# Kernel optimization log

Hardware: AMD Instinct MI355X
Metric: run time of the kernel (lower is better)

Reference implementation:

```python
import jax, jax.numpy as jnp
import numpy as np

C_IN, HIDDEN, C_OUT, N_NODE = 200, 128, 2, 200
BATCH = 512

def setup_inputs() -> dict:
    key = jax.random.key(0)
    k1, k2, k3, k4 = jax.random.split(key, 4)
    x = jax.random.normal(k1, (BATCH, N_NODE, C_IN), dtype=jnp.float32)
    adj = jax.random.randint(k2, (BATCH, N_NODE, N_NODE), 0, 2, dtype=jnp.int32)
    # GINConv MLPs (single Linear each); stored as [in, out]
    W1 = jax.random.normal(k3, (C_IN, HIDDEN), dtype=jnp.float32) / np.sqrt(C_IN)
    b1 = jnp.zeros((HIDDEN,), dtype=jnp.float32)
    W2 = jax.random.normal(k4, (HIDDEN, C_OUT), dtype=jnp.float32) / np.sqrt(HIDDEN)
    b2 = jnp.zeros((C_OUT,), dtype=jnp.float32)
    eps1 = jnp.zeros((), dtype=jnp.float32)  # train_eps=True, init 0
    eps2 = jnp.zeros((), dtype=jnp.float32)
    return {"x": x, "adj": adj, "W1": W1, "b1": b1, "W2": W2, "b2": b2, "eps1": eps1, "eps2": eps2}

def _gin_aggregate(adjf, h):
    # edge (b,i,j) sends h[b,i] to node j: agg[b,j] = sum_i adj[b,i,j]*h[b,i]
    return jnp.einsum('bij,bif->bjf', adjf, h)

def reference(x, adj, W1, b1, W2, b2, eps1, eps2):
    adjf = adj.astype(x.dtype)  # binary 0/1 adjacency [B,N,N]
    # GIN layer 1: nn((1+eps)*x + sum_neighbors(x)), then ReLU
    agg1 = _gin_aggregate(adjf, x)
    h = jax.nn.relu(((1.0 + eps1) * x + agg1) @ W1 + b1)
    # GIN layer 2
    agg2 = _gin_aggregate(adjf, h)
    out = ((1.0 + eps2) * h + agg2) @ W2 + b2  # [B,N,2]
    return out.mean(axis=-2)  # [B,2]
```

## Files before the change

### kernel.cpp

```cpp
#include <hip/hip_runtime.h>

#define BATCH 512
#define NNODE 200
#define CIN   200
#define HID   128
#define IPY   232
#define KCH   7

typedef __attribute__((ext_vector_type(4))) float  f32x4;
typedef __attribute__((ext_vector_type(4))) int    i32x4;
typedef __attribute__((ext_vector_type(8))) short  sh8;
typedef __attribute__((ext_vector_type(4))) short  sh4;
typedef __attribute__((ext_vector_type(8))) __bf16 bf16x8;

__device__ __forceinline__ short f2bf(float x) {
  union { float f; unsigned u; } v; v.f = x;
  unsigned r = v.u + 0x7FFFu + ((v.u >> 16) & 1u);
  return (short)(r >> 16);
}
__device__ __forceinline__ float bf2f(short s) {
  union { unsigned u; float f; } v; v.u = ((unsigned)(unsigned short)s) << 16;
  return v.f;
}
__device__ __forceinline__ f32x4 mfma16(sh8 a, sh8 b, f32x4 c) {
  return __builtin_amdgcn_mfma_f32_16x16x32_bf16(
      __builtin_bit_cast(bf16x8, a), __builtin_bit_cast(bf16x8, b), c, 0, 0, 0);
}
__device__ __forceinline__ f32x4 mfma16i(sh8 a, i32x4 b, f32x4 c) {
  return __builtin_amdgcn_mfma_f32_16x16x32_bf16(
      __builtin_bit_cast(bf16x8, a), __builtin_bit_cast(bf16x8, b), c, 0, 0, 0);
}
__device__ __forceinline__ i32x4 expand8(unsigned byte_) {
  i32x4 w;
#pragma unroll
  for (int h = 0; h < 4; ++h) {
    unsigned p = byte_ >> (2 * h);
    unsigned d = ((p & 1u) ? 0x3F80u : 0u) | ((p & 2u) ? 0x3F800000u : 0u);
    w[h] = (int)d;
  }
  return w;
}

__global__ __launch_bounds__(256) void k_prep(const float* __restrict__ W1,
                                              short* __restrict__ W1T) {
  const int idx = blockIdx.x * 256 + threadIdx.x;
  const int f = idx / IPY, c = idx - f * IPY;
  W1T[idx] = (c < CIN) ? f2bf(W1[(size_t)c * HID + f]) : (short)0;
}

__global__ __launch_bounds__(1024) void k_gin(const float* __restrict__ x,
                                              const int* __restrict__ adj,
                                              const short* __restrict__ W1Tg,
                                              const float* __restrict__ b1,
                                              const float* __restrict__ W2,
                                              const float* __restrict__ b2,
                                              const float* __restrict__ eps1p,
                                              const float* __restrict__ eps2p,
                                              float* __restrict__ out) {
  __shared__ __align__(16) short    ls_w1t[HID * IPY];
  __shared__ __align__(16) short    ls_slab[16 * IPY];
  __shared__ __align__(16) unsigned ls_bits[KCH * 224];
  __shared__ __align__(16) float    ls_deg[224];
  __shared__ __align__(16) float    ls_w2b1[384];
  __shared__               float    ls_part[13][2];

  const int b    = blockIdx.x;
  const int tid  = threadIdx.x;
  const int wave = tid >> 6, lane = tid & 63;
  const int lq   = lane >> 4, lm = lane & 15;
  const int* adjb = adj + (size_t)b * NNODE * NNODE;

  sh8 af[KCH];

  if (wave >= 13) {
    const int iw  = wave - 13;
    const int wd0 = iw * 2, wd1 = (iw == 2) ? 7 : iw * 2 + 2;
    const int jc3 = min(192 + lane, NNODE - 1);
    for (int wd = wd0; wd < wd1; ++wd) {
      const int tmax = (wd == 6) ? 8 : 32;
      unsigned w0 = 0, w1 = 0, w2 = 0, w3 = 0;
      for (int t8 = 0; t8 < tmax; t8 += 8) {
        int v0[8], v1[8], v2[8], v3[8];
#pragma unroll
        for (int rr = 0; rr < 8; ++rr) {
          const int* rp = adjb + (wd * 32 + t8 + rr) * NNODE;
          v0[rr] = rp[lane]; v1[rr] = rp[64 + lane];
          v2[rr] = rp[128 + lane]; v3[rr] = rp[jc3];
        }
#pragma unroll
        for (int rr = 0; rr < 8; ++rr) {
          const int t = t8 + rr;
          const unsigned b0 = (unsigned)v0[rr] & 1u;
          const unsigned b1_ = (unsigned)v1[rr] & 1u;
          const unsigned b2_ = (unsigned)v2[rr] & 1u;
          const unsigned b3_ = (lane < 8) ? ((unsigned)v3[rr] & 1u) : 0u;
          w0 |= b0 << t; w1 |= b1_ << t; w2 |= b2_ << t; w3 |= b3_ << t;
          const int dg = __popcll(__ballot(b0 != 0u)) + __popcll(__ballot(b1_ != 0u))
                       + __popcll(__ballot(b2_ != 0u)) + __popcll(__ballot(b3_ != 0u));
          if (lane == 0) ls_deg[wd * 32 + t] = (float)dg;
        }
      }
      unsigned* bp = &ls_bits[wd * 224];
      bp[lane] = w0; bp[64 + lane] = w1; bp[128 + lane] = w2;
      if (lane < 32) bp[192 + lane] = w3;
    }
  } else {
    sh8 sc[5];
    int chs[5];
#pragma unroll
    for (int it = 0; it < 5; ++it) {
      chs[it] = wave + it * 13;
      if (chs[it] < 58) sc[it] = ((const sh8*)W1Tg)[chs[it] * 64 + lane];
    }
    f32x4 px0[KCH], px1[KCH];
    const int row = min(wave * 16 + lm, NNODE - 1);
    const float* xr = x + (size_t)b * NNODE * CIN + (size_t)row * CIN;
#pragma unroll
    for (int k = 0; k < KCH; ++k) {
      const int c0 = k * 32 + lq * 8;
      f32x4 z = {0.f, 0.f, 0.f, 0.f};
      px0[k] = z; px1[k] = z;
      if (c0 < CIN) { px0[k] = *(const f32x4*)(xr + c0); px1[k] = *(const f32x4*)(xr + c0 + 4); }
    }
    float wv = 0.f;
    if (tid < 384) wv = (tid < 128) ? b1[tid] : W2[tid - 128];
#pragma unroll
    for (int it = 0; it < 5; ++it)
      if (chs[it] < 58) ((sh8*)ls_w1t)[chs[it] * 64 + lane] = sc[it];
    if (tid < 64) {
      const int rw = tid >> 2, p = tid & 3;
      sh8 z = {0, 0, 0, 0, 0, 0, 0, 0};
      *(sh8*)&ls_slab[rw * IPY + 200 + p * 8] = z;
    }
    if (tid < 384) ls_w2b1[tid] = wv;
#pragma unroll
    for (int k = 0; k < KCH; ++k) {
      sh8 a;
#pragma unroll
      for (int jj = 0; jj < 4; ++jj) { a[jj] = f2bf(px0[k][jj]); a[4 + jj] = f2bf(px1[k][jj]); }
      af[k] = a;
    }
  }
  __syncthreads();

  const float e1 = eps1p[0], e2 = eps2p[0];
  const int j = wave * 16 + lm;
  unsigned by[KCH];
  if (wave < 13) {
#pragma unroll
    for (int k = 0; k < KCH; ++k) by[k] = (ls_bits[k * 224 + j] >> (lq * 8)) & 0xFFu;
  }
  float ga = 0.f, gb = 0.f;

  for (int ft = 0; ft < 8; ++ft) {
    const int fb = ft * 16;
    if (wave < 13) {
      const short* wr = &ls_w1t[(fb + lm) * IPY];
      f32x4 acc = {0.f, 0.f, 0.f, 0.f};
#pragma unroll
      for (int k = 0; k < KCH; ++k)
        acc = mfma16(af[k], *(const sh8*)(wr + k * 32 + lq * 8), acc);
      sh4 st;
#pragma unroll
      for (int r = 0; r < 4; ++r) st[r] = f2bf(acc[r]);
      *(sh4*)&ls_slab[lm * IPY + wave * 16 + lq * 4] = st;
    }
    __syncthreads();
    if (wave < 13) {
      const short* yr = &ls_slab[lm * IPY];
      f32x4 accP = {0.f, 0.f, 0.f, 0.f};
#pragma unroll
      for (int k = 0; k < KCH; ++k)
        accP = mfma16i(*(const sh8*)(yr + k * 32 + lq * 8), expand8(by[k]), accP);
#pragma unroll
      for (int r = 0; r < 4; ++r) {
        const int f = fb + lq * 4 + r;
        const float yself = bf2f(ls_slab[(lq * 4 + r) * IPY + j]);
        const float h = fmaxf(accP[r] + (1.f + e1) * yself + ls_w2b1[f], 0.f);
        ga += h * ls_w2b1[128 + 2 * f];
        gb += h * ls_w2b1[129 + 2 * f];
      }
    }
    __syncthreads();
  }

  if (wave < 13) {
    ga += __shfl_xor(ga, 16); ga += __shfl_xor(ga, 32);
    gb += __shfl_xor(gb, 16); gb += __shfl_xor(gb, 32);
    const bool jok = (j < NNODE);
    const float wj = 1.f + e2 + ls_deg[min(j, NNODE - 1)];
    float t0 = jok ? wj * ga : 0.f;
    float t1 = jok ? wj * gb : 0.f;
#pragma unroll
    for (int d = 1; d < 16; d <<= 1) { t0 += __shfl_xor(t0, d); t1 += __shfl_xor(t1, d); }
    if (lane == 0) { ls_part[wave][0] = t0; ls_part[wave][1] = t1; }
  }
  __syncthreads();

  if (tid < 2) {
    float s = 0.f;
#pragma unroll
    for (int q = 0; q < 13; ++q) s += ls_part[q][tid];
    out[b * 2 + tid] = b2[tid] + s * (1.f / NNODE);
  }
}

extern "C" void kernel_launch(void* const* d_in, const int* in_sizes, int n_in,
                              void* d_out, int out_size, void* d_ws, size_t ws_size,
                              hipStream_t stream) {
  const float* x    = (const float*)d_in[0];
  const int*   adj  = (const int*)d_in[1];
  const float* W1   = (const float*)d_in[2];
  const float* b1   = (const float*)d_in[3];
  const float* W2   = (const float*)d_in[4];
  const float* b2   = (const float*)d_in[5];
  const float* eps1 = (const float*)d_in[6];
  const float* eps2 = (const float*)d_in[7];
  float* out = (float*)d_out;

  short* W1T = (short*)d_ws;

  k_prep<<<116, 256, 0, stream>>>(W1, W1T);
  k_gin <<<BATCH, 1024, 0, stream>>>(x, adj, W1T, b1, W2, b2, eps1, eps2, out);
}
```

Measured before the change: 214.8 us.

## Drop LDS W1 staging, read fragment-packed W1 from global, spread adjacency packing

Repacks W1 on the host-side prep kernel into MFMA fragment order so each wave reads its B operand directly from global/L2 instead of staging a 59KB transposed copy in LDS. The block shrinks to 13 waves, and all waves now share the adjacency bit-packing, which is split into 64-column segments with per-segment degree partials that are reduced afterwards. This cuts LDS use, which should allow more blocks per CU, and removes the W1 staging phase. In exchange, every wave reloads W1 fragments from global memory on each feature tile.

```diff
diff --git a/kernel.cpp b/kernel.cpp
--- a/kernel.cpp
+++ b/kernel.cpp
@@ -6,6 +6,7 @@
 #define HID   128
 #define IPY   232
 #define KCH   7
+#define NWAVE 13
 
 typedef __attribute__((ext_vector_type(4))) float  f32x4;
 typedef __attribute__((ext_vector_type(4))) int    i32x4;
@@ -42,27 +43,31 @@
 }
 
 __global__ __launch_bounds__(256) void k_prep(const float* __restrict__ W1,
-                                              short* __restrict__ W1T) {
+                                              short* __restrict__ W1F) {
   const int idx = blockIdx.x * 256 + threadIdx.x;
-  const int f = idx / IPY, c = idx - f * IPY;
-  W1T[idx] = (c < CIN) ? f2bf(W1[(size_t)c * HID + f]) : (short)0;
-}
-
-__global__ __launch_bounds__(1024) void k_gin(const float* __restrict__ x,
-                                              const int* __restrict__ adj,
-                                              const short* __restrict__ W1Tg,
-                                              const float* __restrict__ b1,
-                                              const float* __restrict__ W2,
-                                              const float* __restrict__ b2,
-                                              const float* __restrict__ eps1p,
-                                              const float* __restrict__ eps2p,
-                                              float* __restrict__ out) {
-  __shared__ __align__(16) short    ls_w1t[HID * IPY];
+  const int jj = idx & 7, ln = (idx >> 3) & 63;
+  const int rest = idx >> 9;
+  const int k = rest % 7, ft = rest / 7;
+  const int f = ft * 16 + (ln & 15);
+  const int c = k * 32 + (ln >> 4) * 8 + jj;
+  W1F[idx] = (c < CIN) ? f2bf(W1[(size_t)c * HID + f]) : (short)0;
+}
+
+__global__ __launch_bounds__(832) void k_gin(const float* __restrict__ x,
+                                             const int* __restrict__ adj,
+                                             const short* __restrict__ W1Fg,
+                                             const float* __restrict__ b1,
+                                             const float* __restrict__ W2,
+                                             const float* __restrict__ b2,
+                                             const float* __restrict__ eps1p,
+                                             const float* __restrict__ eps2p,
+                                             float* __restrict__ out) {
   __shared__ __align__(16) short    ls_slab[16 * IPY];
   __shared__ __align__(16) unsigned ls_bits[KCH * 224];
+  __shared__ __align__(16) int      ls_degp[4 * 224];
   __shared__ __align__(16) float    ls_deg[224];
   __shared__ __align__(16) float    ls_w2b1[384];
-  __shared__               float    ls_part[13][2];
+  __shared__               float    ls_part[NWAVE][2];
 
   const int b    = blockIdx.x;
   const int tid  = threadIdx.x;
@@ -70,51 +75,35 @@
   const int lq   = lane >> 4, lm = lane & 15;
   const int* adjb = adj + (size_t)b * NNODE * NNODE;
 
+  float wv = 0.f;
+  if (tid < 384) wv = (tid < 128) ? b1[tid] : W2[tid - 128];
+
+  for (int jb = wave; jb < 28; jb += NWAVE) {
+    const int wd = jb >> 2, seg = jb & 3;
+    const int rmax = (wd == 6) ? 8 : 32;
+    const int j  = seg * 64 + lane;
+    const int jc = min(j, NNODE - 1);
+    const unsigned jv = (j < NNODE) ? 1u : 0u;
+    int v[32];
+#pragma unroll
+    for (int t = 0; t < 32; ++t)
+      v[t] = adjb[(size_t)min(wd * 32 + t, NNODE - 1) * NNODE + jc];
+    unsigned wacc = 0;
+#pragma unroll
+    for (int t = 0; t < 32; ++t) {
+      const unsigned bit = (unsigned)v[t] & jv & (unsigned)(t < rmax ? 1 : 0);
+      wacc |= bit << t;
+      const int dg = __popcll(__ballot(bit != 0u));
+      if (lane == 0 && wd * 32 + t < NNODE) ls_degp[seg * 224 + wd * 32 + t] = dg;
+    }
+    if (j < 224 && (seg < 3 || lane < 32))
+      ls_bits[wd * 224 + j] = wacc;
+  }
+
   sh8 af[KCH];
-
-  if (wave >= 13) {
-    const int iw  = wave - 13;
-    const int wd0 = iw * 2, wd1 = (iw == 2) ? 7 : iw * 2 + 2;
-    const int jc3 = min(192 + lane, NNODE - 1);
-    for (int wd = wd0; wd < wd1; ++wd) {
-      const int tmax = (wd == 6) ? 8 : 32;
-      unsigned w0 = 0, w1 = 0, w2 = 0, w3 = 0;
-      for (int t8 = 0; t8 < tmax; t8 += 8) {
-        int v0[8], v1[8], v2[8], v3[8];
-#pragma unroll
-        for (int rr = 0; rr < 8; ++rr) {
-          const int* rp = adjb + (wd * 32 + t8 + rr) * NNODE;
-          v0[rr] = rp[lane]; v1[rr] = rp[64 + lane];
-          v2[rr] = rp[128 + lane]; v3[rr] = rp[jc3];
-        }
-#pragma unroll
-        for (int rr = 0; rr < 8; ++rr) {
-          const int t = t8 + rr;
-          const unsigned b0 = (unsigned)v0[rr] & 1u;
-          const unsigned b1_ = (unsigned)v1[rr] & 1u;
-          const unsigned b2_ = (unsigned)v2[rr] & 1u;
-          const unsigned b3_ = (lane < 8) ? ((unsigned)v3[rr] & 1u) : 0u;
-          w0 |= b0 << t; w1 |= b1_ << t; w2 |= b2_ << t; w3 |= b3_ << t;
-          const int dg = __popcll(__ballot(b0 != 0u)) + __popcll(__ballot(b1_ != 0u))
-                       + __popcll(__ballot(b2_ != 0u)) + __popcll(__ballot(b3_ != 0u));
-          if (lane == 0) ls_deg[wd * 32 + t] = (float)dg;
-        }
-      }
-      unsigned* bp = &ls_bits[wd * 224];
-      bp[lane] = w0; bp[64 + lane] = w1; bp[128 + lane] = w2;
-      if (lane < 32) bp[192 + lane] = w3;
-    }
-  } else {
-    sh8 sc[5];
-    int chs[5];
-#pragma unroll
-    for (int it = 0; it < 5; ++it) {
-      chs[it] = wave + it * 13;
-      if (chs[it] < 58) sc[it] = ((const sh8*)W1Tg)[chs[it] * 64 + lane];
-    }
+  {
     f32x4 px0[KCH], px1[KCH];
-    const int row = min(wave * 16 + lm, NNODE - 1);
-    const float* xr = x + (size_t)b * NNODE * CIN + (size_t)row * CIN;
+    const float* xr = x + (size_t)b * NNODE * CIN + (size_t)min(wave * 16 + lm, NNODE - 1) * CIN;
 #pragma unroll
     for (int k = 0; k < KCH; ++k) {
       const int c0 = k * 32 + lq * 8;
@@ -122,11 +111,6 @@
       px0[k] = z; px1[k] = z;
       if (c0 < CIN) { px0[k] = *(const f32x4*)(xr + c0); px1[k] = *(const f32x4*)(xr + c0 + 4); }
     }
-    float wv = 0.f;
-    if (tid < 384) wv = (tid < 128) ? b1[tid] : W2[tid - 128];
-#pragma unroll
-    for (int it = 0; it < 5; ++it)
-      if (chs[it] < 58) ((sh8*)ls_w1t)[chs[it] * 64 + lane] = sc[it];
     if (tid < 64) {
       const int rw = tid >> 2, p = tid & 3;
       sh8 z = {0, 0, 0, 0, 0, 0, 0, 0};
@@ -143,30 +127,32 @@
   }
   __syncthreads();
 
+  if (tid < NNODE)
+    ls_deg[tid] = (float)(ls_degp[tid] + ls_degp[224 + tid] +
+                          ls_degp[448 + tid] + ls_degp[672 + tid]);
+
   const float e1 = eps1p[0], e2 = eps2p[0];
   const int j = wave * 16 + lm;
   unsigned by[KCH];
-  if (wave < 13) {
-#pragma unroll
-    for (int k = 0; k < KCH; ++k) by[k] = (ls_bits[k * 224 + j] >> (lq * 8)) & 0xFFu;
-  }
+#pragma unroll
+  for (int k = 0; k < KCH; ++k) by[k] = (ls_bits[k * 224 + j] >> (lq * 8)) & 0xFFu;
   float ga = 0.f, gb = 0.f;
 
   for (int ft = 0; ft < 8; ++ft) {
     const int fb = ft * 16;
-    if (wave < 13) {
-      const short* wr = &ls_w1t[(fb + lm) * IPY];
+    {
+      const sh8* wf = (const sh8*)W1Fg + (size_t)ft * KCH * 64;
       f32x4 acc = {0.f, 0.f, 0.f, 0.f};
 #pragma unroll
       for (int k = 0; k < KCH; ++k)
-        acc = mfma16(af[k], *(const sh8*)(wr + k * 32 + lq * 8), acc);
+        acc = mfma16(af[k], wf[k * 64 + lane], acc);
       sh4 st;
 #pragma unroll
       for (int r = 0; r < 4; ++r) st[r] = f2bf(acc[r]);
       *(sh4*)&ls_slab[lm * IPY + wave * 16 + lq * 4] = st;
     }
     __syncthreads();
-    if (wave < 13) {
+    {
       const short* yr = &ls_slab[lm * IPY];
       f32x4 accP = {0.f, 0.f, 0.f, 0.f};
 #pragma unroll
@@ -184,7 +170,7 @@
     __syncthreads();
   }
 
-  if (wave < 13) {
+  {
     ga += __shfl_xor(ga, 16); ga += __shfl_xor(ga, 32);
     gb += __shfl_xor(gb, 16); gb += __shfl_xor(gb, 32);
     const bool jok = (j < NNODE);
@@ -200,7 +186,7 @@
   if (tid < 2) {
     float s = 0.f;
 #pragma unroll
-    for (int q = 0; q < 13; ++q) s += ls_part[q][tid];
+    for (int q = 0; q < NWAVE; ++q) s += ls_part[q][tid];
     out[b * 2 + tid] = b2[tid] + s * (1.f / NNODE);
   }
 }
@@ -218,8 +204,8 @@
   const float* eps2 = (const float*)d_in[7];
   float* out = (float*)d_out;
 
-  short* W1T = (short*)d_ws;
-
-  k_prep<<<116, 256, 0, stream>>>(W1, W1T);
-  k_gin <<<BATCH, 1024, 0, stream>>>(x, adj, W1T, b1, W2, b2, eps1, eps2, out);
-}
+  short* W1F = (short*)d_ws;
+
+  k_prep<<<112, 256, 0, stream>>>(W1, W1F);
+  k_gin <<<BATCH, NWAVE * 64, 0, stream>>>(x, adj, W1F, b1, W2, b2, eps1, eps2, out);
+}
```

After: 226.2 us. +5.3%, slower.
